# Optimization experiments

Measured on AMD Instinct MI355X. Metric: run time of the kernel, lower is better.

Reference implementation:

```python
import jax, jax.numpy as jnp
import numpy as np

TOPK = 3
RAT_S = 0.05


def _zero_window_mask(h, w, rat_s=RAT_S):
    # mask[src_pixel, tgt_r, tgt_c] = 1 - gauss_r * gauss_c, gaussian centered at src pixel
    sr = h * rat_s
    sc = w * rat_s
    rows = jnp.arange(h, dtype=jnp.float32)
    cols = jnp.arange(w, dtype=jnp.float32)
    gr = jnp.exp(-((rows[None, :] - rows[:, None]) ** 2) / (2.0 * sr * sr))  # (h_src, h_tgt)
    gc = jnp.exp(-((cols[None, :] - cols[:, None]) ** 2) / (2.0 * sc * sc))  # (w_src, w_tgt)
    mask = 1.0 - gr[:, None, :, None] * gc[None, :, None, :]                 # (h,w,h,w)
    return mask.reshape(h * w, h * w)


def setup_inputs() -> dict:
    key = jax.random.key(0)
    b, c, h, w = 2, 256, 64, 64
    x = jax.random.normal(key, (b, c, h, w), dtype=jnp.float32)
    alpha = jnp.float32(5.0)
    return {"x": x, "alpha": alpha}


def reference(x, alpha):
    b, c, h, w = x.shape
    hw = h * w
    # L2-normalize over channels (F.normalize eps=1e-12 uses max(norm, eps))
    nrm = jnp.sqrt(jnp.sum(x * x, axis=1, keepdims=True))
    xn = x / jnp.maximum(nrm, 1e-12)
    xf = xn.reshape(b, c, hw)
    # (b, hw_src, hw_tgt) affinity
    aff = jnp.einsum('bcs,bct->bst', xf, xf)
    mask = _zero_window_mask(h, w)
    x_aff = aff * mask[None]                               # (b, hw, hw)
    logits = x_aff * alpha
    x_c = jax.nn.softmax(logits, axis=-1) * jax.nn.softmax(logits, axis=-2)
    xc_o = x_c.reshape(b, hw, h, w)
    # top-k over source-pixel axis (dim=-3)
    val = jax.lax.top_k(jnp.moveaxis(xc_o, 1, -1), TOPK)[0]  # (b,h,w,k)
    val = jnp.moveaxis(val, -1, 1)                           # (b,k,h,w)
    x_soft = xc_o / (jnp.sum(xc_o, axis=1, keepdims=True) + 1e-8)
    return (val, x_soft)
```

## Files before the change

### kernel.cpp

```cpp
#include <hip/hip_runtime.h>

#define HW 4096
#define CDIM 256
#define BK 32

typedef _Float16 half8 __attribute__((ext_vector_type(8)));
typedef float f32x4 __attribute__((ext_vector_type(4)));

__device__ __forceinline__ void top3_ins(float v, float& a0, float& a1, float& a2) {
  float m01 = fminf(a0, v);
  a0 = fmaxf(a0, v);
  float m12 = fminf(a1, m01);
  a1 = fmaxf(a1, m01);
  a2 = fmaxf(a2, m12);
}

__device__ __forceinline__ float mask_val(const float* gtab, int s, int t) {
  int dr = (s >> 6) - (t >> 6); dr = dr < 0 ? -dr : dr;
  int dc = (s & 63) - (t & 63); dc = dc < 0 ? -dc : dc;
  return 1.0f - gtab[dr] * gtab[dc];
}

__device__ __forceinline__ void async_copy16(const void* g, void* l) {
  __builtin_amdgcn_global_load_lds((const __attribute__((address_space(1))) void*)g,
                                   (__attribute__((address_space(3))) void*)l, 16, 0, 0);
}

__device__ __forceinline__ void stage_slice(const _Float16* __restrict__ X,
                                            int rowBase, int k0,
                                            _Float16* sdst, int w, int lane) {
  const int csrc = ((lane & 3) - ((lane >> 3) & 3)) & 3;
#pragma unroll
  for (int i = 0; i < 2; ++i) {
    const int rchunk = w * 32 + i * 16;
    const _Float16* g =
        X + (size_t)(rowBase + rchunk + (lane >> 2)) * CDIM + k0 + csrc * 8;
    async_copy16(g, sdst + rchunk * BK);
  }
}

__global__ void __launch_bounds__(256) normalize_k(const float* __restrict__ x,
                                                   _Float16* __restrict__ Xf) {
  const int p = threadIdx.x & 31;
  const int g = threadIdx.x >> 5;
  const int P0 = blockIdx.x * 32;
  const int b = P0 >> 12;
  const int ph = (P0 & (HW - 1)) + p;
  const float* xb = x + (size_t)b * CDIM * HW + ph;
  float vals[32];
  float ss = 0.f;
#pragma unroll
  for (int k = 0; k < 32; ++k) {
    float v = xb[(size_t)(g * 32 + k) * HW];
    vals[k] = v;
    ss += v * v;
  }
  __shared__ float ssqp[8][33];
  __shared__ float scl[32];
  ssqp[g][p] = ss;
  __syncthreads();
  if (threadIdx.x < 32) {
    float s2 = 0.f;
#pragma unroll
    for (int gg = 0; gg < 8; ++gg) s2 += ssqp[gg][threadIdx.x];
    scl[threadIdx.x] = 1.0f / fmaxf(sqrtf(s2), 1e-12f);
  }
  __syncthreads();
  const float sc = scl[p];
  _Float16* o = Xf + (size_t)(P0 + p) * CDIM + g * 32;
#pragma unroll
  for (int c8 = 0; c8 < 4; ++c8) {
    half8 h;
#pragma unroll
    for (int j = 0; j < 8; ++j) h[j] = (_Float16)(vals[c8 * 8 + j] * sc);
    *(half8*)(o + c8 * 8) = h;
  }
}

__device__ __forceinline__ void gemm_mainloop(const _Float16* __restrict__ X,
                                              int mBase, int nBase, int lane, int w,
                                              _Float16 (*sA)[128 * BK],
                                              _Float16 (*sB)[128 * BK],
                                              f32x4 (&acc)[4][4]) {
  const int wr = w >> 1, wc = w & 1;
#pragma unroll
  for (int mi = 0; mi < 4; ++mi)
#pragma unroll
    for (int ni = 0; ni < 4; ++ni) acc[mi][ni] = (f32x4){0.f, 0.f, 0.f, 0.f};

  const int aRow0 = wr * 64 + (lane & 15);
  const int bRow0 = wc * 64 + (lane & 15);
  const int cswz = (((lane >> 4) + ((lane >> 1) & 3)) & 3) * 8;

  stage_slice(X, mBase, 0, sA[0], w, lane);
  stage_slice(X, nBase, 0, sB[0], w, lane);

  int cur = 0;
#pragma unroll
  for (int k0 = 0; k0 < CDIM; k0 += BK) {
    __syncthreads();
    if (k0 + BK < CDIM) {
      stage_slice(X, mBase, k0 + BK, sA[cur ^ 1], w, lane);
      stage_slice(X, nBase, k0 + BK, sB[cur ^ 1], w, lane);
    }
    half8 a[4], bfr[4];
#pragma unroll
    for (int i = 0; i < 4; ++i)
      a[i] = *(const half8*)(sA[cur] + (aRow0 + 16 * i) * BK + cswz);
#pragma unroll
    for (int i = 0; i < 4; ++i)
      bfr[i] = *(const half8*)(sB[cur] + (bRow0 + 16 * i) * BK + cswz);
#pragma unroll
    for (int mi = 0; mi < 4; ++mi)
#pragma unroll
      for (int ni = 0; ni < 4; ++ni)
        acc[mi][ni] = __builtin_amdgcn_mfma_f32_16x16x32_f16(a[mi], bfr[ni], acc[mi][ni], 0, 0, 0);
    cur ^= 1;
  }
}

__global__ void __launch_bounds__(256, 3) gemmR_k(const _Float16* __restrict__ Xf,
                                                  const float* __restrict__ alphap,
                                                  float* __restrict__ R) {
  __shared__ _Float16 sA[2][128 * BK];
  __shared__ _Float16 sB[2][128 * BK];
  __shared__ float gtab[64];
  if (threadIdx.x < 64) {
    float d = (float)threadIdx.x;
    gtab[threadIdx.x] = __expf(-d * d * 0.048828125f);
  }
  const float alpha = alphap[0];
  const int b = blockIdx.z;
  const _Float16* X = Xf + (size_t)b * HW * CDIM;
  const int lane = threadIdx.x & 63;
  const int w = threadIdx.x >> 6;
  const int wr = w >> 1, wc = w & 1;
  const int mBase = blockIdx.y * 128;
  const int nBase = blockIdx.x * 128;

  f32x4 acc[4][4];
  gemm_mainloop(X, mBase, nBase, lane, w, sA, sB, acc);

  const int quad = lane >> 4;
  float csum[4] = {0.f, 0.f, 0.f, 0.f};
#pragma unroll
  for (int mi = 0; mi < 4; ++mi) {
#pragma unroll
    for (int r = 0; r < 4; ++r) {
      const int s = mBase + wr * 64 + mi * 16 + quad * 4 + r;
#pragma unroll
      for (int ni = 0; ni < 4; ++ni) {
        const int t = nBase + wc * 64 + ni * 16 + (lane & 15);
        csum[ni] += __expf(alpha * mask_val(gtab, s, t) * acc[mi][ni][r]);
      }
    }
  }
#pragma unroll
  for (int off = 16; off < 64; off <<= 1)
#pragma unroll
    for (int ni = 0; ni < 4; ++ni) csum[ni] += __shfl_xor(csum[ni], off);
  if (quad == 0) {
#pragma unroll
    for (int ni = 0; ni < 4; ++ni)
      atomicAdd(&R[b * HW + nBase + wc * 64 + ni * 16 + (lane & 15)], csum[ni]);
  }
}

__global__ void __launch_bounds__(256, 3) gemmT_k(const _Float16* __restrict__ Xf,
                                                  const float* __restrict__ alphap,
                                                  const float* __restrict__ R,
                                                  float* __restrict__ part) {
  __shared__ _Float16 sA[2][128 * BK];
  __shared__ _Float16 sB[2][128 * BK];
  __shared__ float gtab[64];
  __shared__ float sRinv[128];
  __shared__ float sStats[2][128][4];
  const int b = blockIdx.z;
  const int mBase = blockIdx.y * 128;
  const int nBase = blockIdx.x * 128;
  if (threadIdx.x < 64) {
    float d = (float)threadIdx.x;
    gtab[threadIdx.x] = __expf(-d * d * 0.048828125f);
  }
  if (threadIdx.x < 128)
    sRinv[threadIdx.x] = 1.0f / R[b * HW + mBase + threadIdx.x];
  const float alpha = alphap[0];
  const _Float16* X = Xf + (size_t)b * HW * CDIM;
  const int lane = threadIdx.x & 63;
  const int w = threadIdx.x >> 6;
  const int wr = w >> 1, wc = w & 1;

  f32x4 acc[4][4];
  gemm_mainloop(X, mBase, nBase, lane, w, sA, sB, acc);

  const int quad = lane >> 4;
  float tsum[4] = {0.f, 0.f, 0.f, 0.f};
  float q0[4] = {0.f, 0.f, 0.f, 0.f}, q1[4] = {0.f, 0.f, 0.f, 0.f}, q2[4] = {0.f, 0.f, 0.f, 0.f};
#pragma unroll
  for (int mi = 0; mi < 4; ++mi) {
#pragma unroll
    for (int r = 0; r < 4; ++r) {
      const int lrow = wr * 64 + mi * 16 + quad * 4 + r;
      const int s = mBase + lrow;
      const float inv = sRinv[lrow];
#pragma unroll
      for (int ni = 0; ni < 4; ++ni) {
        const int t = nBase + wc * 64 + ni * 16 + (lane & 15);
        float e = __expf(alpha * mask_val(gtab, s, t) * acc[mi][ni][r]);
        float g = e * e * inv;
        tsum[ni] += g;
        top3_ins(g, q0[ni], q1[ni], q2[ni]);
      }
    }
  }
#pragma unroll
  for (int off = 16; off < 64; off <<= 1) {
#pragma unroll
    for (int ni = 0; ni < 4; ++ni) {
      tsum[ni] += __shfl_xor(tsum[ni], off);
      float b0 = __shfl_xor(q0[ni], off);
      float b1 = __shfl_xor(q1[ni], off);
      float b2 = __shfl_xor(q2[ni], off);
      top3_ins(b0, q0[ni], q1[ni], q2[ni]);
      top3_ins(b1, q0[ni], q1[ni], q2[ni]);
      top3_ins(b2, q0[ni], q1[ni], q2[ni]);
    }
  }
  if (quad == 0) {
#pragma unroll
    for (int ni = 0; ni < 4; ++ni) {
      const int col = wc * 64 + ni * 16 + (lane & 15);
      sStats[wr][col][0] = tsum[ni];
      sStats[wr][col][1] = q0[ni];
      sStats[wr][col][2] = q1[ni];
      sStats[wr][col][3] = q2[ni];
    }
  }
  __syncthreads();
  if (threadIdx.x < 128) {
    float su = sStats[0][threadIdx.x][0] + sStats[1][threadIdx.x][0];
    float a0 = sStats[0][threadIdx.x][1];
    float a1 = sStats[0][threadIdx.x][2];
    float a2 = sStats[0][threadIdx.x][3];
    top3_ins(sStats[1][threadIdx.x][1], a0, a1, a2);
    top3_ins(sStats[1][threadIdx.x][2], a0, a1, a2);
    top3_ins(sStats[1][threadIdx.x][3], a0, a1, a2);
    f32x4 o = {su, a0, a1, a2};
    *(f32x4*)(part + ((size_t)(b * 32 + blockIdx.y) * HW + nBase + threadIdx.x) * 4) = o;
  }
}

__global__ void __launch_bounds__(256) merge_k(const float* __restrict__ R,
                                               const float* __restrict__ part,
                                               float* __restrict__ W,
                                               float* __restrict__ val_out) {
  const int idx = blockIdx.x * 256 + threadIdx.x;
  const int b = idx >> 12;
  const int t = idx & (HW - 1);
  float T = 0.f, a0 = 0.f, a1 = 0.f, a2 = 0.f;
#pragma unroll 8
  for (int sblk = 0; sblk < 32; ++sblk) {
    f32x4 p = *(const f32x4*)(part + ((size_t)(b * 32 + sblk) * HW + t) * 4);
    T += p[0];
    top3_ins(p[1], a0, a1, a2);
    top3_ins(p[2], a0, a1, a2);
    top3_ins(p[3], a0, a1, a2);
  }
  const float r = R[idx];
  const float invr = 1.0f / r;
  val_out[(b * 3 + 0) * HW + t] = a0 * invr;
  val_out[(b * 3 + 1) * HW + t] = a1 * invr;
  val_out[(b * 3 + 2) * HW + t] = a2 * invr;
  W[idx] = 1.0f / (T + 1e-8f * r);
}

__global__ void __launch_bounds__(256, 3) gemmW_k(const _Float16* __restrict__ Xf,
                                                  const float* __restrict__ alphap,
                                                  const float* __restrict__ R,
                                                  const float* __restrict__ W,
                                                  float* __restrict__ outX) {
  __shared__ _Float16 sA[2][128 * BK];
  __shared__ _Float16 sB[2][128 * BK];
  __shared__ float gtab[64];
  __shared__ float sRinv[128];
  __shared__ float sWc[128];
  const int b = blockIdx.z;
  const int mBase = blockIdx.y * 128;
  const int nBase = blockIdx.x * 128;
  if (threadIdx.x < 64) {
    float d = (float)threadIdx.x;
    gtab[threadIdx.x] = __expf(-d * d * 0.048828125f);
  }
  if (threadIdx.x < 128) {
    sRinv[threadIdx.x] = 1.0f / R[b * HW + mBase + threadIdx.x];
    sWc[threadIdx.x] = W[b * HW + nBase + threadIdx.x];
  }
  const float alpha = alphap[0];
  const _Float16* X = Xf + (size_t)b * HW * CDIM;
  const int lane = threadIdx.x & 63;
  const int w = threadIdx.x >> 6;
  const int wr = w >> 1, wc = w & 1;

  f32x4 acc[4][4];
  gemm_mainloop(X, mBase, nBase, lane, w, sA, sB, acc);

  const int quad = lane >> 4;
  float* Xb = outX + (size_t)b * HW * HW;
#pragma unroll
  for (int mi = 0; mi < 4; ++mi) {
#pragma unroll
    for (int r = 0; r < 4; ++r) {
      const int lrow = wr * 64 + mi * 16 + quad * 4 + r;
      const int s = mBase + lrow;
      const float inv = sRinv[lrow];
      float* orow = Xb + (size_t)s * HW;
#pragma unroll
      for (int ni = 0; ni < 4; ++ni) {
        const int col = wc * 64 + ni * 16 + (lane & 15);
        const int t = nBase + col;
        float e = __expf(alpha * mask_val(gtab, s, t) * acc[mi][ni][r]);
        orow[t] = e * e * inv * sWc[col];
      }
    }
  }
}

extern "C" void kernel_launch(void* const* d_in, const int* in_sizes, int n_in,
                              void* d_out, int out_size, void* d_ws, size_t ws_size,
                              hipStream_t stream) {
  const float* x = (const float*)d_in[0];
  const float* alphap = (const float*)d_in[1];
  float* out = (float*)d_out;
  float* out_val = out;
  float* out_x = out + 2 * 3 * HW;
  char* ws = (char*)d_ws;

  _Float16* Xf = (_Float16*)ws;
  float* R = (float*)(ws + (size_t)4194304);
  float* W = R + 2 * HW;
  float* part = out_x;

  hipMemsetAsync(R, 0, (size_t)2 * HW * sizeof(float), stream);

  normalize_k<<<dim3(256), dim3(256), 0, stream>>>(x, Xf);
  gemmR_k<<<dim3(32, 32, 2), dim3(256), 0, stream>>>(Xf, alphap, R);
  gemmT_k<<<dim3(32, 32, 2), dim3(256), 0, stream>>>(Xf, alphap, R, part);
  merge_k<<<dim3(32), dim3(256), 0, stream>>>(R, part, W, out_val);
  gemmW_k<<<dim3(32, 32, 2), dim3(256), 0, stream>>>(Xf, alphap, R, W, out_x);
}
```

Measured before the change: 224.7 us.

## Exploit affinity symmetry: compute only upper-triangular tiles in R and T passes

The affinity matrix and the mask are both symmetric, so gemmR_k and gemmT_k now launch only the 528 upper-triangular 128x128 tiles per batch, mapped from a linear block index. Each off-diagonal tile also produces row-wise sums and top-3 statistics for the mirrored tile, using the transposed normalizer. This roughly halves the GEMM and exp work in these two passes. In exchange the epilogue gets extra shuffles, atomics and shared memory, which may lower occupancy.

```diff
diff --git a/kernel.cpp b/kernel.cpp
--- a/kernel.cpp
+++ b/kernel.cpp
@@ -19,6 +19,14 @@
   int dr = (s >> 6) - (t >> 6); dr = dr < 0 ? -dr : dr;
   int dc = (s & 63) - (t & 63); dc = dc < 0 ? -dc : dc;
   return 1.0f - gtab[dr] * gtab[dc];
+}
+
+__device__ __forceinline__ void tri_map(int L, int& i, int& j) {
+  int jj = (int)((sqrtf(8.f * (float)L + 1.f) - 1.f) * 0.5f);
+  while ((jj + 1) * (jj + 2) / 2 <= L) ++jj;
+  while (jj * (jj + 1) / 2 > L) --jj;
+  j = jj;
+  i = L - jj * (jj + 1) / 2;
 }
 
 __device__ __forceinline__ void async_copy16(const void* g, void* l) {
@@ -129,29 +137,41 @@
     float d = (float)threadIdx.x;
     gtab[threadIdx.x] = __expf(-d * d * 0.048828125f);
   }
+  int iT, jT;
+  tri_map(blockIdx.x, iT, jT);
+  const int mBase = iT * 128;
+  const int nBase = jT * 128;
   const float alpha = alphap[0];
   const int b = blockIdx.z;
   const _Float16* X = Xf + (size_t)b * HW * CDIM;
   const int lane = threadIdx.x & 63;
   const int w = threadIdx.x >> 6;
   const int wr = w >> 1, wc = w & 1;
-  const int mBase = blockIdx.y * 128;
-  const int nBase = blockIdx.x * 128;
 
   f32x4 acc[4][4];
   gemm_mainloop(X, mBase, nBase, lane, w, sA, sB, acc);
 
   const int quad = lane >> 4;
+  const bool offd = (iT != jT);
+  float* Rb = R + b * HW;
   float csum[4] = {0.f, 0.f, 0.f, 0.f};
 #pragma unroll
   for (int mi = 0; mi < 4; ++mi) {
 #pragma unroll
     for (int r = 0; r < 4; ++r) {
       const int s = mBase + wr * 64 + mi * 16 + quad * 4 + r;
+      float rsum = 0.f;
 #pragma unroll
       for (int ni = 0; ni < 4; ++ni) {
         const int t = nBase + wc * 64 + ni * 16 + (lane & 15);
-        csum[ni] += __expf(alpha * mask_val(gtab, s, t) * acc[mi][ni][r]);
+        float e = __expf(alpha * mask_val(gtab, s, t) * acc[mi][ni][r]);
+        csum[ni] += e;
+        rsum += e;
+      }
+      if (offd) {
+#pragma unroll
+        for (int off = 1; off < 16; off <<= 1) rsum += __shfl_xor(rsum, off);
+        if ((lane & 15) == 0) atomicAdd(&Rb[s], rsum);
       }
     }
   }
@@ -162,7 +182,7 @@
   if (quad == 0) {
 #pragma unroll
     for (int ni = 0; ni < 4; ++ni)
-      atomicAdd(&R[b * HW + nBase + wc * 64 + ni * 16 + (lane & 15)], csum[ni]);
+      atomicAdd(&Rb[nBase + wc * 64 + ni * 16 + (lane & 15)], csum[ni]);
   }
 }
 
@@ -173,17 +193,23 @@
   __shared__ _Float16 sA[2][128 * BK];
   __shared__ _Float16 sB[2][128 * BK];
   __shared__ float gtab[64];
-  __shared__ float sRinv[128];
-  __shared__ float sStats[2][128][4];
+  __shared__ float sRinvM[128];
+  __shared__ float sRinvN[128];
+  __shared__ float colStats[2][128][4];
+  __shared__ float rowStats[2][128][4];
+  int iT, jT;
+  tri_map(blockIdx.x, iT, jT);
+  const int mBase = iT * 128;
+  const int nBase = jT * 128;
   const int b = blockIdx.z;
-  const int mBase = blockIdx.y * 128;
-  const int nBase = blockIdx.x * 128;
   if (threadIdx.x < 64) {
     float d = (float)threadIdx.x;
     gtab[threadIdx.x] = __expf(-d * d * 0.048828125f);
   }
-  if (threadIdx.x < 128)
-    sRinv[threadIdx.x] = 1.0f / R[b * HW + mBase + threadIdx.x];
+  if (threadIdx.x < 128) {
+    sRinvM[threadIdx.x] = 1.0f / R[b * HW + mBase + threadIdx.x];
+    sRinvN[threadIdx.x] = 1.0f / R[b * HW + nBase + threadIdx.x];
+  }
   const float alpha = alphap[0];
   const _Float16* X = Xf + (size_t)b * HW * CDIM;
   const int lane = threadIdx.x & 63;
@@ -194,6 +220,7 @@
   gemm_mainloop(X, mBase, nBase, lane, w, sA, sB, acc);
 
   const int quad = lane >> 4;
+  const bool offd = (iT != jT);
   float tsum[4] = {0.f, 0.f, 0.f, 0.f};
   float q0[4] = {0.f, 0.f, 0.f, 0.f}, q1[4] = {0.f, 0.f, 0.f, 0.f}, q2[4] = {0.f, 0.f, 0.f, 0.f};
 #pragma unroll
@@ -202,14 +229,38 @@
     for (int r = 0; r < 4; ++r) {
       const int lrow = wr * 64 + mi * 16 + quad * 4 + r;
       const int s = mBase + lrow;
-      const float inv = sRinv[lrow];
+      const float invm = sRinvM[lrow];
+      float rsum = 0.f, r0 = 0.f, r1 = 0.f, r2 = 0.f;
 #pragma unroll
       for (int ni = 0; ni < 4; ++ni) {
-        const int t = nBase + wc * 64 + ni * 16 + (lane & 15);
+        const int lcol = wc * 64 + ni * 16 + (lane & 15);
+        const int t = nBase + lcol;
         float e = __expf(alpha * mask_val(gtab, s, t) * acc[mi][ni][r]);
-        float g = e * e * inv;
+        float e2 = e * e;
+        float g = e2 * invm;
         tsum[ni] += g;
         top3_ins(g, q0[ni], q1[ni], q2[ni]);
+        if (offd) {
+          float gm = e2 * sRinvN[lcol];
+          rsum += gm;
+          top3_ins(gm, r0, r1, r2);
+        }
+      }
+      if (offd) {
+#pragma unroll
+        for (int off = 1; off < 16; off <<= 1) {
+          rsum += __shfl_xor(rsum, off);
+          float b0 = __shfl_xor(r0, off);
+          float b1 = __shfl_xor(r1, off);
+          float b2 = __shfl_xor(r2, off);
+          top3_ins(b0, r0, r1, r2);
+          top3_ins(b1, r0, r1, r2);
+          top3_ins(b2, r0, r1, r2);
+        }
+        if ((lane & 15) == 0) {
+          f32x4 o = {rsum, r0, r1, r2};
+          *(f32x4*)&rowStats[wc][lrow][0] = o;
+        }
       }
     }
   }
@@ -230,23 +281,35 @@
 #pragma unroll
     for (int ni = 0; ni < 4; ++ni) {
       const int col = wc * 64 + ni * 16 + (lane & 15);
-      sStats[wr][col][0] = tsum[ni];
-      sStats[wr][col][1] = q0[ni];
-      sStats[wr][col][2] = q1[ni];
-      sStats[wr][col][3] = q2[ni];
+      f32x4 o = {tsum[ni], q0[ni], q1[ni], q2[ni]};
+      *(f32x4*)&colStats[wr][col][0] = o;
     }
   }
   __syncthreads();
   if (threadIdx.x < 128) {
-    float su = sStats[0][threadIdx.x][0] + sStats[1][threadIdx.x][0];
-    float a0 = sStats[0][threadIdx.x][1];
-    float a1 = sStats[0][threadIdx.x][2];
-    float a2 = sStats[0][threadIdx.x][3];
-    top3_ins(sStats[1][threadIdx.x][1], a0, a1, a2);
-    top3_ins(sStats[1][threadIdx.x][2], a0, a1, a2);
-    top3_ins(sStats[1][threadIdx.x][3], a0, a1, a2);
-    f32x4 o = {su, a0, a1, a2};
-    *(f32x4*)(part + ((size_t)(b * 32 + blockIdx.y) * HW + nBase + threadIdx.x) * 4) = o;
+    const int tid = threadIdx.x;
+    {
+      float su = colStats[0][tid][0] + colStats[1][tid][0];
+      float a0 = colStats[0][tid][1];
+      float a1 = colStats[0][tid][2];
+      float a2 = colStats[0][tid][3];
+      top3_ins(colStats[1][tid][1], a0, a1, a2);
+      top3_ins(colStats[1][tid][2], a0, a1, a2);
+      top3_ins(colStats[1][tid][3], a0, a1, a2);
+      f32x4 o = {su, a0, a1, a2};
+      *(f32x4*)(part + ((size_t)(b * 32 + iT) * HW + nBase + tid) * 4) = o;
+    }
+    if (offd) {
+      float su = rowStats[0][tid][0] + rowStats[1][tid][0];
+      float a0 = rowStats[0][tid][1];
+      float a1 = rowStats[0][tid][2];
+      float a2 = rowStats[0][tid][3];
+      top3_ins(rowStats[1][tid][1], a0, a1, a2);
+      top3_ins(rowStats[1][tid][2], a0, a1, a2);
+      top3_ins(rowStats[1][tid][3], a0, a1, a2);
+      f32x4 o = {su, a0, a1, a2};
+      *(f32x4*)(part + ((size_t)(b * 32 + jT) * HW + mBase + tid) * 4) = o;
+    }
   }
 }
 
@@ -343,8 +406,8 @@
   hipMemsetAsync(R, 0, (size_t)2 * HW * sizeof(float), stream);
 
   normalize_k<<<dim3(256), dim3(256), 0, stream>>>(x, Xf);
-  gemmR_k<<<dim3(32, 32, 2), dim3(256), 0, stream>>>(Xf, alphap, R);
-  gemmT_k<<<dim3(32, 32, 2), dim3(256), 0, stream>>>(Xf, alphap, R, part);
+  gemmR_k<<<dim3(528, 1, 2), dim3(256), 0, stream>>>(Xf, alphap, R);
+  gemmT_k<<<dim3(528, 1, 2), dim3(256), 0, stream>>>(Xf, alphap, R, part);
   merge_k<<<dim3(32), dim3(256), 0, stream>>>(R, part, W, out_val);
   gemmW_k<<<dim3(32, 32, 2), dim3(256), 0, stream>>>(Xf, alphap, R, W, out_x);
 }
```

Result: slower. 238.3 us (+6.1%).
